# Optimization experiments

Hardware: AMD Instinct MI355X
Metric: run time of the kernel (lower is better)

Reference implementation:

```python
import jax, jax.numpy as jnp
import numpy as np

MIN_NORM = 1e-15
BALL_EPS = 4e-3   # float32 boundary eps (HGCN PoincareBall convention)
ATANH_EPS = 1e-7  # artanh clamp margin safe in fp32 (orig 1e-15 in fp64)
C = 1.0           # curvature


def _norm(x):
    return jnp.clip(jnp.linalg.norm(x, axis=-1, keepdims=True), MIN_NORM, None)


def artanh(x):
    x = jnp.clip(x, -1.0 + ATANH_EPS, 1.0 - ATANH_EPS)
    return 0.5 * (jnp.log1p(x) - jnp.log1p(-x))


def proj(x, c):
    norm = _norm(x)
    maxnorm = (1.0 - BALL_EPS) / jnp.sqrt(c)
    return jnp.where(norm > maxnorm, x / norm * maxnorm, x)


def expmap0(u, c):
    sqrt_c = jnp.sqrt(c)
    u_norm = _norm(u)
    return jnp.tanh(sqrt_c * u_norm) * u / (sqrt_c * u_norm)


def logmap0(p, c):
    sqrt_c = jnp.sqrt(c)
    p_norm = _norm(p)
    return artanh(sqrt_c * p_norm) * p / (sqrt_c * p_norm)


def mobius_add(x, y, c):
    x2 = jnp.sum(x * x, axis=-1, keepdims=True)
    y2 = jnp.sum(y * y, axis=-1, keepdims=True)
    xy = jnp.sum(x * y, axis=-1, keepdims=True)
    num = (1.0 + 2.0 * c * xy + c * y2) * x + (1.0 - c * x2) * y
    denom = 1.0 + 2.0 * c * xy + c * c * x2 * y2
    return num / jnp.clip(denom, MIN_NORM, None)


def mobius_matvec(W, x, c):
    # W: [out, in], x: [N, in]
    sqrt_c = jnp.sqrt(c)
    x_norm = _norm(x)
    mx = x @ W.T                      # [N, out]
    mx_norm = _norm(mx)
    res_c = jnp.tanh(mx_norm / x_norm * artanh(sqrt_c * x_norm)) * mx / (mx_norm * sqrt_c)
    cond = jnp.all(mx == 0.0, axis=-1, keepdims=True)
    return jnp.where(cond, 0.0, res_c)


def setup_inputs() -> dict:
    key = jax.random.key(0)
    k1, k2 = jax.random.split(key)
    N, din, dout = 524288, 128, 128
    # points on the Poincare ball: expmap0 of small tangent vectors
    u = 0.1 * jax.random.normal(k1, (N, din), dtype=jnp.float32)
    x = proj(expmap0(u, C), C)
    # xavier_uniform with gain=sqrt(2)
    bound = np.sqrt(2.0) * np.sqrt(6.0 / (din + dout))
    W = jax.random.uniform(k2, (dout, din), dtype=jnp.float32, minval=-bound, maxval=bound)
    b = jnp.zeros((dout,), dtype=jnp.float32)
    return {"x": x, "W": W, "b": b}


def reference(x, W, b):
    # dropout p=0 / eval -> identity on W
    res = proj(mobius_matvec(W, x, C), C)
    # proj_tan0 is identity on the Poincare ball
    hyp_bias = proj(expmap0(b[None, :], C), C)
    res = proj(mobius_add(res, hyp_bias, C), C)
    # nonlinearity in tangent space at origin
    res = jax.nn.relu(logmap0(res, C))
    res = proj(expmap0(res, C), C)
    return res
```

## Files before the change

kernel.cpp:

```cpp
#include <hip/hip_runtime.h>

typedef __attribute__((ext_vector_type(8))) short short8;
typedef __attribute__((ext_vector_type(4))) float f32x4;

#define MAXNORM 0.996f
#define MINNORM 1e-15f
#define ATEPS   (1.0f - 1e-7f)

__device__ __forceinline__ float frcp(float x) { return __builtin_amdgcn_rcpf(x); }
__device__ __forceinline__ float artanh_c(float z) {
    z = fminf(z, ATEPS);
    return 0.5f * __logf((1.0f + z) * frcp(1.0f - z));
}
__device__ __forceinline__ float tanh_pos(float a) {
    float e = __expf(-2.0f * a);
    return (1.0f - e) * frcp(1.0f + e);
}
__device__ __forceinline__ unsigned short f2bf(float f) {
    union { float f; unsigned u; } v; v.f = f;
    unsigned r = v.u + 0x7FFFu + ((v.u >> 16) & 1u);
    return (unsigned short)(r >> 16);
}

__global__ __launch_bounds__(256) void blinear_kernel(
    const float* __restrict__ Xf,
    const float* __restrict__ Wf,
    const float* __restrict__ Bf,
    float* __restrict__ Out)
{
    const int lane = threadIdx.x & 63;
    const int wave = threadIdx.x >> 6;
    const int c = lane & 15;
    const int q = lane >> 4;
    const long rowbase = (long)blockIdx.x * 128 + wave * 32;

    float b0 = Bf[lane];
    float b1 = Bf[64 + lane];
    float bn2 = b0 * b0 + b1 * b1;
    #pragma unroll
    for (int m = 1; m <= 32; m <<= 1) bn2 += __shfl_xor(bn2, m);
    float bn = fmaxf(sqrtf(bn2), MINNORM);
    float tb = tanh_pos(bn);
    float fb = fminf(tb, MAXNORM) * frcp(bn);
    float hb2 = fb * fb * bn2;
    float hbv[8];
    #pragma unroll
    for (int nt = 0; nt < 8; ++nt) hbv[nt] = fb * Bf[nt * 16 + c];

    short8 afr[2][4];
    float xq[2] = {0.0f, 0.0f};
    #pragma unroll
    for (int t = 0; t < 2; ++t) {
        const float* xrow = Xf + (rowbase + t * 16 + c) * 128;
        #pragma unroll
        for (int ks = 0; ks < 4; ++ks) {
            f32x4 a0 = *(const f32x4*)(xrow + ks * 32 + q * 8);
            f32x4 a1 = *(const f32x4*)(xrow + ks * 32 + q * 8 + 4);
            short8 s;
            #pragma unroll
            for (int j = 0; j < 4; ++j) {
                float v0 = a0[j], v1 = a1[j];
                xq[t] = fmaf(v0, v0, fmaf(v1, v1, xq[t]));
                s[j] = (short)f2bf(v0);
                s[4 + j] = (short)f2bf(v1);
            }
            afr[t][ks] = s;
        }
    }
    #pragma unroll
    for (int t = 0; t < 2; ++t) { xq[t] += __shfl_xor(xq[t], 16); xq[t] += __shfl_xor(xq[t], 32); }
    float xn2v[2][4];
    #pragma unroll
    for (int t = 0; t < 2; ++t)
        #pragma unroll
        for (int r = 0; r < 4; ++r) xn2v[t][r] = __shfl(xq[t], q * 4 + r);

    f32x4 acc[2][8];
    {
        f32x4 z = {0.0f, 0.0f, 0.0f, 0.0f};
        #pragma unroll
        for (int t = 0; t < 2; ++t)
            #pragma unroll
            for (int nt = 0; nt < 8; ++nt) acc[t][nt] = z;
    }
    #pragma unroll
    for (int nt = 0; nt < 8; ++nt) {
        const float* wrow = Wf + (nt * 16 + c) * 128;
        #pragma unroll
        for (int ks = 0; ks < 4; ++ks) {
            f32x4 w0 = *(const f32x4*)(wrow + ks * 32 + q * 8);
            f32x4 w1 = *(const f32x4*)(wrow + ks * 32 + q * 8 + 4);
            short8 bfr;
            #pragma unroll
            for (int j = 0; j < 4; ++j) {
                bfr[j] = (short)f2bf(w0[j]);
                bfr[4 + j] = (short)f2bf(w1[j]);
            }
            acc[0][nt] = __builtin_amdgcn_mfma_f32_16x16x32_bf16(afr[0][ks], bfr, acc[0][nt], 0, 0, 0);
            acc[1][nt] = __builtin_amdgcn_mfma_f32_16x16x32_bf16(afr[1][ks], bfr, acc[1][nt], 0, 0, 0);
        }
    }

    float mn2[2][4] = {}, mhb[2][4] = {};
    #pragma unroll
    for (int t = 0; t < 2; ++t)
        #pragma unroll
        for (int nt = 0; nt < 8; ++nt)
            #pragma unroll
            for (int r = 0; r < 4; ++r) {
                float v = acc[t][nt][r];
                mn2[t][r] = fmaf(v, v, mn2[t][r]);
                mhb[t][r] = fmaf(v, hbv[nt], mhb[t][r]);
            }
    #pragma unroll
    for (int m = 1; m <= 8; m <<= 1)
        #pragma unroll
        for (int t = 0; t < 2; ++t)
            #pragma unroll
            for (int r = 0; r < 4; ++r) {
                mn2[t][r] += __shfl_xor(mn2[t][r], m);
                mhb[t][r] += __shfl_xor(mhb[t][r], m);
            }

    float A1[2][4], B1[2][4], Gg[2][4], S3[2][4];
    #pragma unroll
    for (int t = 0; t < 2; ++t)
        #pragma unroll
        for (int r = 0; r < 4; ++r) {
            float xn = fmaxf(sqrtf(xn2v[t][r]), MINNORM);
            float mn = fmaxf(sqrtf(mn2[t][r]), MINNORM);
            float t1 = tanh_pos(mn * frcp(xn) * artanh_c(xn));
            float rn = fminf(t1, MAXNORM);
            float f1 = rn * frcp(mn);
            float x2 = rn * rn;
            float xy = f1 * mhb[t][r];
            float Aa = 1.0f + 2.0f * xy + hb2;
            float Bb = 1.0f - x2;
            float Dn = fmaxf(1.0f + 2.0f * xy + x2 * hb2, MINNORM);
            float rD = frcp(Dn);
            float a1 = Aa * f1 * rD;
            float b1_ = Bb * rD;
            float r2n2 = a1 * a1 * mn2[t][r] + 2.0f * a1 * b1_ * mhb[t][r] + b1_ * b1_ * hb2;
            float r2n = sqrtf(fmaxf(r2n2, 0.0f));
            float g = (r2n > MAXNORM) ? (MAXNORM * frcp(r2n)) : 1.0f;
            float n3 = fmaxf(fminf(r2n, MAXNORM), MINNORM);
            float s3 = artanh_c(n3) * frcp(n3);
            A1[t][r] = a1; B1[t][r] = b1_; Gg[t][r] = g; S3[t][r] = s3;
        }

    float q2[2][4] = {};
    #pragma unroll
    for (int t = 0; t < 2; ++t)
        #pragma unroll
        for (int nt = 0; nt < 8; ++nt)
            #pragma unroll
            for (int r = 0; r < 4; ++r) {
                float v = fmaf(A1[t][r], acc[t][nt][r], B1[t][r] * hbv[nt]);
                v = fmaxf(v, 0.0f);
                acc[t][nt][r] = v;
                q2[t][r] = fmaf(v, v, q2[t][r]);
            }
    #pragma unroll
    for (int m = 1; m <= 8; m <<= 1)
        #pragma unroll
        for (int t = 0; t < 2; ++t)
            #pragma unroll
            for (int r = 0; r < 4; ++r) q2[t][r] += __shfl_xor(q2[t][r], m);

    float K[2][4];
    #pragma unroll
    for (int t = 0; t < 2; ++t)
        #pragma unroll
        for (int r = 0; r < 4; ++r) {
            float sg = S3[t][r] * Gg[t][r];
            float tn_t = sg * sqrtf(q2[t][r]);
            float tn = fmaxf(tn_t, MINNORM);
            float t4 = tanh_pos(tn);
            K[t][r] = fminf(t4, MAXNORM) * frcp(tn) * sg;
        }

    #pragma unroll
    for (int t = 0; t < 2; ++t)
        #pragma unroll
        for (int r = 0; r < 4; ++r) {
            long row = rowbase + t * 16 + q * 4 + r;
            float* orow = Out + row * 128;
            #pragma unroll
            for (int nt = 0; nt < 8; ++nt)
                orow[nt * 16 + c] = K[t][r] * acc[t][nt][r];
        }
}

extern "C" void kernel_launch(void* const* d_in, const int* in_sizes, int n_in,
                              void* d_out, int out_size, void* d_ws, size_t ws_size,
                              hipStream_t stream) {
    const float* X = (const float*)d_in[0];
    const float* W = (const float*)d_in[1];
    const float* B = (const float*)d_in[2];
    float* Out = (float*)d_out;
    const int N = in_sizes[0] / 128;
    const int blocks = N / 128;
    blinear_kernel<<<blocks, 256, 0, stream>>>(X, W, B, Out);
}
```

Before: 514.4 us.

## Prepack W to bf16 fragments, use packed bf16 convert, skip zero-bias work

Adds a small pre-kernel that converts W into bf16 MFMA-fragment order in workspace, so each block loads ready fragments instead of reconverting W. X conversion uses the hardware v_cvt_pk_bf16_f32 instruction instead of manual rounding. The bias dot-product reduction and bias add are skipped when the hyperbolic bias norm is zero, and launch bounds now request 4 blocks per CU. Bias skipping is a runtime branch, still correct for nonzero bias, but it is the path the zero-bias test input takes.

```diff
diff --git a/kernel.cpp b/kernel.cpp
--- a/kernel.cpp
+++ b/kernel.cpp
@@ -2,6 +2,7 @@
 
 typedef __attribute__((ext_vector_type(8))) short short8;
 typedef __attribute__((ext_vector_type(4))) float f32x4;
+typedef __attribute__((ext_vector_type(4))) unsigned int u32x4;
 
 #define MAXNORM 0.996f
 #define MINNORM 1e-15f
@@ -21,10 +22,33 @@
     unsigned r = v.u + 0x7FFFu + ((v.u >> 16) & 1u);
     return (unsigned short)(r >> 16);
 }
-
-__global__ __launch_bounds__(256) void blinear_kernel(
+__device__ __forceinline__ unsigned cvt_pk_bf16(float lo, float hi) {
+    unsigned r;
+    asm("v_cvt_pk_bf16_f32 %0, %1, %2" : "=v"(r) : "v"(lo), "v"(hi));
+    return r;
+}
+
+__global__ __launch_bounds__(256) void wpack_kernel(
+    const float* __restrict__ Wf, short8* __restrict__ Wp)
+{
+    const int tid = blockIdx.x * 256 + threadIdx.x;
+    const int l = tid & 63;
+    const int f = tid >> 6;
+    const int nt = f >> 2, ks = f & 3;
+    const int c = l & 15, q = l >> 4;
+    const float* src = Wf + (nt * 16 + c) * 128 + ks * 32 + q * 8;
+    short8 s;
+    #pragma unroll
+    for (int j = 0; j < 4; ++j) {
+        s[j]     = (short)f2bf(src[j]);
+        s[4 + j] = (short)f2bf(src[4 + j]);
+    }
+    Wp[tid] = s;
+}
+
+__global__ __launch_bounds__(256, 4) void blinear_kernel(
     const float* __restrict__ Xf,
-    const float* __restrict__ Wf,
+    const short8* __restrict__ Wp,
     const float* __restrict__ Bf,
     float* __restrict__ Out)
 {
@@ -56,15 +80,15 @@
         for (int ks = 0; ks < 4; ++ks) {
             f32x4 a0 = *(const f32x4*)(xrow + ks * 32 + q * 8);
             f32x4 a1 = *(const f32x4*)(xrow + ks * 32 + q * 8 + 4);
-            short8 s;
-            #pragma unroll
-            for (int j = 0; j < 4; ++j) {
-                float v0 = a0[j], v1 = a1[j];
-                xq[t] = fmaf(v0, v0, fmaf(v1, v1, xq[t]));
-                s[j] = (short)f2bf(v0);
-                s[4 + j] = (short)f2bf(v1);
-            }
-            afr[t][ks] = s;
+            #pragma unroll
+            for (int j = 0; j < 4; ++j)
+                xq[t] = fmaf(a0[j], a0[j], fmaf(a1[j], a1[j], xq[t]));
+            union { u32x4 u; short8 s; } cv;
+            cv.u[0] = cvt_pk_bf16(a0[0], a0[1]);
+            cv.u[1] = cvt_pk_bf16(a0[2], a0[3]);
+            cv.u[2] = cvt_pk_bf16(a1[0], a1[1]);
+            cv.u[3] = cvt_pk_bf16(a1[2], a1[3]);
+            afr[t][ks] = cv.s;
         }
     }
     #pragma unroll
@@ -85,17 +109,9 @@
     }
     #pragma unroll
     for (int nt = 0; nt < 8; ++nt) {
-        const float* wrow = Wf + (nt * 16 + c) * 128;
         #pragma unroll
         for (int ks = 0; ks < 4; ++ks) {
-            f32x4 w0 = *(const f32x4*)(wrow + ks * 32 + q * 8);
-            f32x4 w1 = *(const f32x4*)(wrow + ks * 32 + q * 8 + 4);
-            short8 bfr;
-            #pragma unroll
-            for (int j = 0; j < 4; ++j) {
-                bfr[j] = (short)f2bf(w0[j]);
-                bfr[4 + j] = (short)f2bf(w1[j]);
-            }
+            short8 bfr = Wp[(nt * 4 + ks) * 64 + lane];
             acc[0][nt] = __builtin_amdgcn_mfma_f32_16x16x32_bf16(afr[0][ks], bfr, acc[0][nt], 0, 0, 0);
             acc[1][nt] = __builtin_amdgcn_mfma_f32_16x16x32_bf16(afr[1][ks], bfr, acc[1][nt], 0, 0, 0);
         }
@@ -110,19 +126,30 @@
             for (int r = 0; r < 4; ++r) {
                 float v = acc[t][nt][r];
                 mn2[t][r] = fmaf(v, v, mn2[t][r]);
-                mhb[t][r] = fmaf(v, hbv[nt], mhb[t][r]);
             }
     #pragma unroll
     for (int m = 1; m <= 8; m <<= 1)
         #pragma unroll
         for (int t = 0; t < 2; ++t)
             #pragma unroll
-            for (int r = 0; r < 4; ++r) {
-                mn2[t][r] += __shfl_xor(mn2[t][r], m);
-                mhb[t][r] += __shfl_xor(mhb[t][r], m);
-            }
-
-    float A1[2][4], B1[2][4], Gg[2][4], S3[2][4];
+            for (int r = 0; r < 4; ++r) mn2[t][r] += __shfl_xor(mn2[t][r], m);
+    if (hb2 != 0.0f) {
+        #pragma unroll
+        for (int t = 0; t < 2; ++t)
+            #pragma unroll
+            for (int nt = 0; nt < 8; ++nt)
+                #pragma unroll
+                for (int r = 0; r < 4; ++r)
+                    mhb[t][r] = fmaf(acc[t][nt][r], hbv[nt], mhb[t][r]);
+        #pragma unroll
+        for (int m = 1; m <= 8; m <<= 1)
+            #pragma unroll
+            for (int t = 0; t < 2; ++t)
+                #pragma unroll
+                for (int r = 0; r < 4; ++r) mhb[t][r] += __shfl_xor(mhb[t][r], m);
+    }
+
+    float A1[2][4], B1[2][4], SG[2][4];
     #pragma unroll
     for (int t = 0; t < 2; ++t)
         #pragma unroll
@@ -145,21 +172,34 @@
             float g = (r2n > MAXNORM) ? (MAXNORM * frcp(r2n)) : 1.0f;
             float n3 = fmaxf(fminf(r2n, MAXNORM), MINNORM);
             float s3 = artanh_c(n3) * frcp(n3);
-            A1[t][r] = a1; B1[t][r] = b1_; Gg[t][r] = g; S3[t][r] = s3;
+            A1[t][r] = a1; B1[t][r] = b1_; SG[t][r] = s3 * g;
         }
 
     float q2[2][4] = {};
-    #pragma unroll
-    for (int t = 0; t < 2; ++t)
-        #pragma unroll
-        for (int nt = 0; nt < 8; ++nt)
-            #pragma unroll
-            for (int r = 0; r < 4; ++r) {
-                float v = fmaf(A1[t][r], acc[t][nt][r], B1[t][r] * hbv[nt]);
-                v = fmaxf(v, 0.0f);
-                acc[t][nt][r] = v;
-                q2[t][r] = fmaf(v, v, q2[t][r]);
-            }
+    if (hb2 != 0.0f) {
+        #pragma unroll
+        for (int t = 0; t < 2; ++t)
+            #pragma unroll
+            for (int nt = 0; nt < 8; ++nt)
+                #pragma unroll
+                for (int r = 0; r < 4; ++r) {
+                    float v = fmaf(A1[t][r], acc[t][nt][r], B1[t][r] * hbv[nt]);
+                    v = fmaxf(v, 0.0f);
+                    acc[t][nt][r] = v;
+                    q2[t][r] = fmaf(v, v, q2[t][r]);
+                }
+    } else {
+        #pragma unroll
+        for (int t = 0; t < 2; ++t)
+            #pragma unroll
+            for (int nt = 0; nt < 8; ++nt)
+                #pragma unroll
+                for (int r = 0; r < 4; ++r) {
+                    float v = fmaxf(A1[t][r] * acc[t][nt][r], 0.0f);
+                    acc[t][nt][r] = v;
+                    q2[t][r] = fmaf(v, v, q2[t][r]);
+                }
+    }
     #pragma unroll
     for (int m = 1; m <= 8; m <<= 1)
         #pragma unroll
@@ -172,7 +212,7 @@
     for (int t = 0; t < 2; ++t)
         #pragma unroll
         for (int r = 0; r < 4; ++r) {
-            float sg = S3[t][r] * Gg[t][r];
+            float sg = SG[t][r];
             float tn_t = sg * sqrtf(q2[t][r]);
             float tn = fmaxf(tn_t, MINNORM);
             float t4 = tanh_pos(tn);
@@ -198,7 +238,8 @@
     const float* W = (const float*)d_in[1];
     const float* B = (const float*)d_in[2];
     float* Out = (float*)d_out;
+    short8* Wp = (short8*)d_ws;
     const int N = in_sizes[0] / 128;
-    const int blocks = N / 128;
-    blinear_kernel<<<blocks, 256, 0, stream>>>(X, W, B, Out);
-}
+    wpack_kernel<<<8, 256, 0, stream>>>(W, Wp);
+    blinear_kernel<<<N / 128, 256, 0, stream>>>(X, Wp, B, Out);
+}
```

After: 543.0 us. 1.06x slower.
